# Kernel optimization log

Hardware: AMD Instinct MI355X
Metric: run time of the kernel (lower is better)

Reference implementation:

```python
import jax, jax.numpy as jnp
import numpy as np

DX = 1000.0
DY = 1000.0
EPS = 1e-8


def _weno5(qm2, qm1, q0, qp1, qp2):
    """Classic WENO5 left-biased reconstruction at the face i+1/2."""
    # candidate stencil reconstructions
    f1 = (1.0 / 3.0) * qm2 - (7.0 / 6.0) * qm1 + (11.0 / 6.0) * q0
    f2 = -(1.0 / 6.0) * qm1 + (5.0 / 6.0) * q0 + (1.0 / 3.0) * qp1
    f3 = (1.0 / 3.0) * q0 + (5.0 / 6.0) * qp1 - (1.0 / 6.0) * qp2
    # smoothness indicators
    k1, k2 = 13.0 / 12.0, 0.25
    b1 = k1 * (qm2 - 2.0 * qm1 + q0) ** 2 + k2 * (qm2 - 4.0 * qm1 + 3.0 * q0) ** 2
    b2 = k1 * (qm1 - 2.0 * q0 + qp1) ** 2 + k2 * (qm1 - qp1) ** 2
    b3 = k1 * (q0 - 2.0 * qp1 + qp2) ** 2 + k2 * (3.0 * q0 - 4.0 * qp1 + qp2) ** 2
    # nonlinear weights (ideal weights 1/10, 6/10, 3/10)
    w1 = 0.1 / (b1 + EPS) ** 2
    w2 = 0.6 / (b2 + EPS) ** 2
    w3 = 0.3 / (b3 + EPS) ** 2
    return (w1 * f1 + w2 * f2 + w3 * f3) / (w1 + w2 + w3)


def _flux_along(q, vel, axis):
    """Upwind WENO5 flux vel * q_face at faces i+1/2, one face per cell.

    fe[..., i] = flux at face between cells i and i+1 along `axis`.
    Boundary stencils use edge-replicated ghost cells.
    """
    n = q.shape[axis]
    pad = [(0, 0), (0, 0)]
    pad[axis] = (2, 3)  # left recon needs i-2..i+2, right recon needs i-1..i+3
    qp = jnp.pad(q, pad, mode='edge')

    def s(k):  # q at cell i+k, shape == q.shape
        return jax.lax.slice_in_dim(qp, 2 + k, 2 + k + n, axis=axis)

    q_left = _weno5(s(-2), s(-1), s(0), s(1), s(2))   # upwind for vel >= 0
    q_right = _weno5(s(3), s(2), s(1), s(0), s(-1))   # upwind for vel <  0 (mirrored)
    return vel * jnp.where(vel >= 0.0, q_left, q_right)


def setup_inputs() -> dict:
    key = jax.random.key(0)
    k1, k2, k3 = jax.random.split(key, 3)
    Ny, Nx = 2048, 4096
    h = jax.random.normal(k1, (Ny, Nx), dtype=jnp.float32)
    u = jax.random.normal(k2, (Ny, Nx), dtype=jnp.float32)
    v = jax.random.normal(k3, (Ny, Nx), dtype=jnp.float32)
    return {"h": h, "u": u, "v": v}


def reference(h, u, v):
    # WENO5 upwind fluxes at east (U-point) and north (V-point) faces
    fe = _flux_along(h, u, axis=1)
    fn = _flux_along(h, v, axis=0)
    # tendency -div(h u_vec) on the ghost=2 interior, zero on the ghost ring
    div = (fe[2:-2, 2:-2] - fe[2:-2, 1:-3]) / DX + (fn[2:-2, 2:-2] - fn[1:-3, 2:-2]) / DY
    out = jnp.zeros_like(h).at[2:-2, 2:-2].set(-div)
    return out
```

## Files before the change

kernel.cpp:

```cpp
#include <hip/hip_runtime.h>

#define NX 4096
#define NY 2048
#define EPS 1e-8f
#define ROWS 8
#define CPW 63
#define INV_D 0.001f

typedef float f32x2 __attribute__((ext_vector_type(2)));

__device__ __forceinline__ int clampi(int i, int lo, int hi) {
    return i < lo ? lo : (i > hi ? hi : i);
}

__device__ __forceinline__ float weno5_s(float qm2, float qm1, float q0,
                                         float qp1, float qp2) {
    float f1 = fmaf(1.0f/3.0f, qm2, fmaf(-7.0f/6.0f, qm1, (11.0f/6.0f)*q0));
    float f2 = fmaf(-1.0f/6.0f, qm1, fmaf(5.0f/6.0f, q0, (1.0f/3.0f)*qp1));
    float f3 = fmaf(1.0f/3.0f, q0, fmaf(5.0f/6.0f, qp1, (-1.0f/6.0f)*qp2));
    const float k1 = 13.0f/12.0f, k2 = 0.25f;
    float d1 = qm2 - 2.0f*qm1 + q0,  e1 = qm2 - 4.0f*qm1 + 3.0f*q0;
    float d2 = qm1 - 2.0f*q0 + qp1,  e2 = qm1 - qp1;
    float d3 = q0 - 2.0f*qp1 + qp2,  e3 = 3.0f*q0 - 4.0f*qp1 + qp2;
    float b1 = fmaf(k1, d1*d1, k2*(e1*e1));
    float b2 = fmaf(k1, d2*d2, k2*(e2*e2));
    float b3 = fmaf(k1, d3*d3, k2*(e3*e3));
    float t1 = b1 + EPS, t2 = b2 + EPS, t3 = b3 + EPS;
    float p23 = t2*t3, p13 = t1*t3, p12 = t1*t2;
    float w1 = 0.1f*(p23*p23), w2 = 0.6f*(p13*p13), w3 = 0.3f*(p12*p12);
    float num = fmaf(w1, f1, fmaf(w2, f2, w3*f3));
    return num * __builtin_amdgcn_rcpf((w1 + w2) + w3);
}

__device__ __forceinline__ f32x2 weno5_pk(f32x2 qm2, f32x2 qm1, f32x2 q0,
                                          f32x2 qp1, f32x2 qp2) {
    f32x2 f1 = (1.0f/3.0f)*qm2 - (7.0f/6.0f)*qm1 + (11.0f/6.0f)*q0;
    f32x2 f2 = (-1.0f/6.0f)*qm1 + (5.0f/6.0f)*q0 + (1.0f/3.0f)*qp1;
    f32x2 f3 = (1.0f/3.0f)*q0 + (5.0f/6.0f)*qp1 - (1.0f/6.0f)*qp2;
    f32x2 d1 = qm2 - 2.0f*qm1 + q0;
    f32x2 e1 = qm2 - 4.0f*qm1 + 3.0f*q0;
    f32x2 d2 = qm1 - 2.0f*q0 + qp1;
    f32x2 e2 = qm1 - qp1;
    f32x2 d3 = q0 - 2.0f*qp1 + qp2;
    f32x2 e3 = 3.0f*q0 - 4.0f*qp1 + qp2;
    const float k1 = 13.0f/12.0f, k2 = 0.25f;
    f32x2 b1 = k1*(d1*d1) + k2*(e1*e1);
    f32x2 b2 = k1*(d2*d2) + k2*(e2*e2);
    f32x2 b3 = k1*(d3*d3) + k2*(e3*e3);
    f32x2 t1 = b1 + EPS, t2 = b2 + EPS, t3 = b3 + EPS;
    f32x2 p23 = t2*t3, p13 = t1*t3, p12 = t1*t2;
    f32x2 w1 = 0.1f*(p23*p23);
    f32x2 w2 = 0.6f*(p13*p13);
    f32x2 w3 = 0.3f*(p12*p12);
    f32x2 num = w1*f1 + w2*f2 + w3*f3;
    f32x2 den = (w1 + w2) + w3;
    f32x2 rc;
    rc.x = __builtin_amdgcn_rcpf(den.x);
    rc.y = __builtin_amdgcn_rcpf(den.y);
    return num * rc;
}

template <bool EDGE>
__device__ __forceinline__ void run_strip(const float* __restrict__ h,
                                          const float* __restrict__ u,
                                          const float* __restrict__ v,
                                          float* __restrict__ out,
                                          int x0, int y0w, int lane) {
    const int xf = x0 - 1 + lane;
    const int xo = x0 + lane;
    const int xc = EDGE ? (xo < NX ? xo : NX - 1) : xo;
    const int xq = EDGE ? clampi(xf, 0, NX - 1) : xf;

    int xs[6];
    if (EDGE) {
#pragma unroll
        for (int k = 0; k < 6; ++k) xs[k] = clampi(xf - 2 + k, 0, NX - 1);
    }

    float col[ROWS + 6];
#pragma unroll
    for (int k = 0; k < ROWS + 6; ++k) {
        int yy = EDGE ? clampi(y0w - 3 + k, 0, NY - 1) : (y0w - 3 + k);
        col[k] = h[(size_t)yy * NX + xc];
    }
    float uu[ROWS];
#pragma unroll
    for (int r = 0; r < ROWS; ++r)
        uu[r] = u[(size_t)(y0w + r) * NX + xq];
    float vv[ROWS + 1];
#pragma unroll
    for (int j = 0; j <= ROWS; ++j) {
        int fy = EDGE ? clampi(y0w - 1 + j, 0, NY - 1) : (y0w - 1 + j);
        vv[j] = v[(size_t)fy * NX + xc];
    }
    float st[ROWS][6];
#pragma unroll
    for (int r = 0; r < ROWS; ++r) {
        const float* hr = h + (size_t)(y0w + r) * NX;
        if (EDGE) {
#pragma unroll
            for (int k = 0; k < 6; ++k) st[r][k] = hr[xs[k]];
        } else {
#pragma unroll
            for (int k = 0; k < 6; ++k) st[r][k] = hr[xf - 2 + k];
        }
    }

    float fn_prev;
    {
        float vl = vv[0];
        bool vp = (vl >= 0.0f);
        fn_prev = vl * weno5_s(vp ? col[0] : col[5], vp ? col[1] : col[4],
                               vp ? col[2] : col[3], vp ? col[3] : col[2],
                               vp ? col[4] : col[1]);
    }

#pragma unroll
    for (int r = 0; r < ROWS; ++r) {
        const int y = y0w + r;
        float uval = uu[r];
        float vval = vv[r + 1];
        bool up = (uval >= 0.0f);
        bool vp = (vval >= 0.0f);
        f32x2 a = { up ? st[r][0] : st[r][5], vp ? col[r+1] : col[r+6] };
        f32x2 b = { up ? st[r][1] : st[r][4], vp ? col[r+2] : col[r+5] };
        f32x2 c = { up ? st[r][2] : st[r][3], vp ? col[r+3] : col[r+4] };
        f32x2 d = { up ? st[r][3] : st[r][2], vp ? col[r+4] : col[r+3] };
        f32x2 e = { up ? st[r][4] : st[r][1], vp ? col[r+5] : col[r+2] };
        f32x2 q = weno5_pk(a, b, c, d, e);
        float fe = uval * q.x;
        float fn_cur = vval * q.y;
        float fe_r = __shfl_down(fe, 1);
        float val = ((fe - fe_r) + (fn_prev - fn_cur)) * INV_D;

        if (EDGE) {
            if (xo < 2 || xo >= NX - 2 || y < 2 || y >= NY - 2) val = 0.0f;
            if (lane < CPW && xo < NX)
                __builtin_nontemporal_store(val, out + (size_t)y * NX + xo);
        } else {
            if (lane < CPW)
                __builtin_nontemporal_store(val, out + (size_t)y * NX + xo);
        }
        fn_prev = fn_cur;
    }
}

__global__ __launch_bounds__(256) void adv_kernel(const float* __restrict__ h,
                                                  const float* __restrict__ u,
                                                  const float* __restrict__ v,
                                                  float* __restrict__ out) {
    const int lane = threadIdx.x & 63;
    const int wid  = threadIdx.x >> 6;
    const int x0 = blockIdx.x * CPW;
    const int y0w = (blockIdx.y * 4 + wid) * ROWS;

    const bool edge = (blockIdx.x == 0) || (blockIdx.x >= 64) ||
                      (blockIdx.y == 0) || (blockIdx.y == gridDim.y - 1);
    if (edge)
        run_strip<true>(h, u, v, out, x0, y0w, lane);
    else
        run_strip<false>(h, u, v, out, x0, y0w, lane);
}

extern "C" void kernel_launch(void* const* d_in, const int* in_sizes, int n_in,
                              void* d_out, int out_size, void* d_ws, size_t ws_size,
                              hipStream_t stream) {
    const float* h = (const float*)d_in[0];
    const float* u = (const float*)d_in[1];
    const float* v = (const float*)d_in[2];
    float* out = (float*)d_out;

    dim3 block(256, 1, 1);
    dim3 grid((NX + CPW - 1) / CPW, NY / (4 * ROWS), 1);
    adv_kernel<<<grid, block, 0, stream>>>(h, u, v, out);
}
```

Before: 38.88 us.

## Pair WENO evaluations by direction and software-pipeline row stencil loads

Replaces the old pairing, where each packed WENO call combined one x-face and one y-face, with same-direction pairs: all y-face fluxes are computed up front in packed pairs, and x-face fluxes are computed two rows at a time. Row stencil and u loads are double-buffered so the loads for the next row pair are issued while the current pair is being computed, instead of all loads landing before any compute. The aim is to hide memory latency and to cut the select logic needed per packed call. In exchange, register pressure may rise because all y fluxes are held in registers, and instruction scheduling changes.

```diff
diff --git a/kernel.cpp b/kernel.cpp
--- a/kernel.cpp
+++ b/kernel.cpp
@@ -77,71 +77,108 @@
         for (int k = 0; k < 6; ++k) xs[k] = clampi(xf - 2 + k, 0, NX - 1);
     }
 
-    float col[ROWS + 6];
+    float w[ROWS + 6];
 #pragma unroll
     for (int k = 0; k < ROWS + 6; ++k) {
         int yy = EDGE ? clampi(y0w - 3 + k, 0, NY - 1) : (y0w - 3 + k);
-        col[k] = h[(size_t)yy * NX + xc];
-    }
-    float uu[ROWS];
-#pragma unroll
-    for (int r = 0; r < ROWS; ++r)
-        uu[r] = u[(size_t)(y0w + r) * NX + xq];
+        w[k] = h[(size_t)yy * NX + xc];
+    }
     float vv[ROWS + 1];
 #pragma unroll
     for (int j = 0; j <= ROWS; ++j) {
         int fy = EDGE ? clampi(y0w - 1 + j, 0, NY - 1) : (y0w - 1 + j);
         vv[j] = v[(size_t)fy * NX + xc];
     }
-    float st[ROWS][6];
-#pragma unroll
-    for (int r = 0; r < ROWS; ++r) {
-        const float* hr = h + (size_t)(y0w + r) * NX;
+
+    float st[4][2][6];
+    float uu[4][2];
+
+#pragma unroll
+    for (int i = 0; i < 2; ++i) {
+        const float* hr = h + (size_t)(y0w + i) * NX;
         if (EDGE) {
 #pragma unroll
-            for (int k = 0; k < 6; ++k) st[r][k] = hr[xs[k]];
+            for (int k = 0; k < 6; ++k) st[0][i][k] = hr[xs[k]];
         } else {
 #pragma unroll
-            for (int k = 0; k < 6; ++k) st[r][k] = hr[xf - 2 + k];
+            for (int k = 0; k < 6; ++k) st[0][i][k] = hr[xf - 2 + k];
         }
-    }
-
-    float fn_prev;
+        uu[0][i] = u[(size_t)(y0w + i) * NX + xq];
+    }
+
+    float fn[ROWS + 1];
+#pragma unroll
+    for (int j = 0; j < ROWS; j += 2) {
+        float v0 = vv[j], v1 = vv[j + 1];
+        bool p0 = (v0 >= 0.0f), p1 = (v1 >= 0.0f);
+        f32x2 a = { p0 ? w[j]   : w[j+5], p1 ? w[j+1] : w[j+6] };
+        f32x2 b = { p0 ? w[j+1] : w[j+4], p1 ? w[j+2] : w[j+5] };
+        f32x2 c = { p0 ? w[j+2] : w[j+3], p1 ? w[j+3] : w[j+4] };
+        f32x2 d = { p0 ? w[j+3] : w[j+2], p1 ? w[j+4] : w[j+3] };
+        f32x2 e = { p0 ? w[j+4] : w[j+1], p1 ? w[j+5] : w[j+2] };
+        f32x2 q = weno5_pk(a, b, c, d, e);
+        fn[j] = v0 * q.x;
+        fn[j + 1] = v1 * q.y;
+    }
     {
-        float vl = vv[0];
+        float vl = vv[ROWS];
         bool vp = (vl >= 0.0f);
-        fn_prev = vl * weno5_s(vp ? col[0] : col[5], vp ? col[1] : col[4],
-                               vp ? col[2] : col[3], vp ? col[3] : col[2],
-                               vp ? col[4] : col[1]);
-    }
-
-#pragma unroll
-    for (int r = 0; r < ROWS; ++r) {
-        const int y = y0w + r;
-        float uval = uu[r];
-        float vval = vv[r + 1];
-        bool up = (uval >= 0.0f);
-        bool vp = (vval >= 0.0f);
-        f32x2 a = { up ? st[r][0] : st[r][5], vp ? col[r+1] : col[r+6] };
-        f32x2 b = { up ? st[r][1] : st[r][4], vp ? col[r+2] : col[r+5] };
-        f32x2 c = { up ? st[r][2] : st[r][3], vp ? col[r+3] : col[r+4] };
-        f32x2 d = { up ? st[r][3] : st[r][2], vp ? col[r+4] : col[r+3] };
-        f32x2 e = { up ? st[r][4] : st[r][1], vp ? col[r+5] : col[r+2] };
+        fn[ROWS] = vl * weno5_s(vp ? w[ROWS]   : w[ROWS+5],
+                                vp ? w[ROWS+1] : w[ROWS+4],
+                                vp ? w[ROWS+2] : w[ROWS+3],
+                                vp ? w[ROWS+3] : w[ROWS+2],
+                                vp ? w[ROWS+4] : w[ROWS+1]);
+    }
+
+#pragma unroll
+    for (int p = 0; p < 4; ++p) {
+        if (p < 3) {
+#pragma unroll
+            for (int i = 0; i < 2; ++i) {
+                int y = y0w + 2 * (p + 1) + i;
+                const float* hr = h + (size_t)y * NX;
+                if (EDGE) {
+#pragma unroll
+                    for (int k = 0; k < 6; ++k) st[p+1][i][k] = hr[xs[k]];
+                } else {
+#pragma unroll
+                    for (int k = 0; k < 6; ++k) st[p+1][i][k] = hr[xf - 2 + k];
+                }
+                uu[p+1][i] = u[(size_t)y * NX + xq];
+            }
+        }
+
+        float u0 = uu[p][0], u1 = uu[p][1];
+        bool q0p = (u0 >= 0.0f), q1p = (u1 >= 0.0f);
+        f32x2 a = { q0p ? st[p][0][0] : st[p][0][5], q1p ? st[p][1][0] : st[p][1][5] };
+        f32x2 b = { q0p ? st[p][0][1] : st[p][0][4], q1p ? st[p][1][1] : st[p][1][4] };
+        f32x2 c = { q0p ? st[p][0][2] : st[p][0][3], q1p ? st[p][1][2] : st[p][1][3] };
+        f32x2 d = { q0p ? st[p][0][3] : st[p][0][2], q1p ? st[p][1][3] : st[p][1][2] };
+        f32x2 e = { q0p ? st[p][0][4] : st[p][0][1], q1p ? st[p][1][4] : st[p][1][1] };
         f32x2 q = weno5_pk(a, b, c, d, e);
-        float fe = uval * q.x;
-        float fn_cur = vval * q.y;
-        float fe_r = __shfl_down(fe, 1);
-        float val = ((fe - fe_r) + (fn_prev - fn_cur)) * INV_D;
-
+        float fe0 = u0 * q.x;
+        float fe1 = u1 * q.y;
+        float fe0r = __shfl_down(fe0, 1);
+        float fe1r = __shfl_down(fe1, 1);
+
+        int r0 = 2 * p;
+        float val0 = ((fe0 - fe0r) + (fn[r0]     - fn[r0 + 1])) * INV_D;
+        float val1 = ((fe1 - fe1r) + (fn[r0 + 1] - fn[r0 + 2])) * INV_D;
+
+        int y0r = y0w + r0;
         if (EDGE) {
-            if (xo < 2 || xo >= NX - 2 || y < 2 || y >= NY - 2) val = 0.0f;
-            if (lane < CPW && xo < NX)
-                __builtin_nontemporal_store(val, out + (size_t)y * NX + xo);
+            if (xo < 2 || xo >= NX - 2 || y0r < 2 || y0r >= NY - 2) val0 = 0.0f;
+            if (xo < 2 || xo >= NX - 2 || y0r + 1 < 2 || y0r + 1 >= NY - 2) val1 = 0.0f;
+            if (lane < CPW && xo < NX) {
+                __builtin_nontemporal_store(val0, out + (size_t)y0r * NX + xo);
+                __builtin_nontemporal_store(val1, out + (size_t)(y0r + 1) * NX + xo);
+            }
         } else {
-            if (lane < CPW)
-                __builtin_nontemporal_store(val, out + (size_t)y * NX + xo);
+            if (lane < CPW) {
+                __builtin_nontemporal_store(val0, out + (size_t)y0r * NX + xo);
+                __builtin_nontemporal_store(val1, out + (size_t)(y0r + 1) * NX + xo);
+            }
         }
-        fn_prev = fn_cur;
     }
 }
 
```

After: 39.24 us. No clear change (+0.9%).

## Load interior h row once per lane and build x-stencil with cross-lane shuffles

Applied to the files above, without the earlier changes.

The interior path now loads a single h value per lane per row (offset by three columns) and builds the six-point x-stencil and the center column from wavefront shuffles, replacing six separate global loads per row. To keep enough halo lanes for the shifted window, columns per wave drop from 63 to 56, and the edge predicate is updated to match. This cuts load instructions and cache traffic in exchange for more shuffle (ds_bpermute) work and a larger grid with more redundant halo lanes.

```diff
diff --git a/kernel.cpp b/kernel.cpp
--- a/kernel.cpp
+++ b/kernel.cpp
@@ -4,7 +4,7 @@
 #define NY 2048
 #define EPS 1e-8f
 #define ROWS 8
-#define CPW 63
+#define CPW 56
 #define INV_D 0.001f
 
 typedef float f32x2 __attribute__((ext_vector_type(2)));
@@ -60,50 +60,114 @@
     return num * rc;
 }
 
-template <bool EDGE>
-__device__ __forceinline__ void run_strip(const float* __restrict__ h,
-                                          const float* __restrict__ u,
-                                          const float* __restrict__ v,
-                                          float* __restrict__ out,
-                                          int x0, int y0w, int lane) {
+__device__ __forceinline__ void run_int(const float* __restrict__ h,
+                                        const float* __restrict__ u,
+                                        const float* __restrict__ v,
+                                        float* __restrict__ out,
+                                        int x0, int y0w, int lane) {
+    const int xh = x0 - 3 + lane;
+    const int xq = x0 - 1 + lane;
+    const int xc = x0 + lane;
+
+    float hv[ROWS];
+#pragma unroll
+    for (int r = 0; r < ROWS; ++r)
+        hv[r] = h[(size_t)(y0w + r) * NX + xh];
+    float col[ROWS + 6];
+#pragma unroll
+    for (int k = 0; k < 3; ++k) {
+        col[k] = h[(size_t)(y0w - 3 + k) * NX + xc];
+        col[ROWS + 3 + k] = h[(size_t)(y0w + ROWS + k) * NX + xc];
+    }
+    float uu[ROWS];
+#pragma unroll
+    for (int r = 0; r < ROWS; ++r)
+        uu[r] = u[(size_t)(y0w + r) * NX + xq];
+    float vv[ROWS + 1];
+#pragma unroll
+    for (int j = 0; j <= ROWS; ++j)
+        vv[j] = v[(size_t)(y0w - 1 + j) * NX + xc];
+
+#pragma unroll
+    for (int r = 0; r < ROWS; ++r)
+        col[3 + r] = __shfl(hv[r], lane + 3);
+
+    float fn_prev;
+    {
+        float vl = vv[0];
+        bool vp = (vl >= 0.0f);
+        fn_prev = vl * weno5_s(vp ? col[0] : col[5], vp ? col[1] : col[4],
+                               vp ? col[2] : col[3], vp ? col[3] : col[2],
+                               vp ? col[4] : col[1]);
+    }
+
+#pragma unroll
+    for (int r = 0; r < ROWS; ++r) {
+        const int y = y0w + r;
+        float s0 = hv[r];
+        float s1 = __shfl(hv[r], lane + 1);
+        float s2 = __shfl(hv[r], lane + 2);
+        float s3 = col[r + 3];
+        float s4 = __shfl(hv[r], lane + 4);
+        float s5 = __shfl(hv[r], lane + 5);
+
+        float uval = uu[r];
+        float vval = vv[r + 1];
+        bool up = (uval >= 0.0f);
+        bool vp = (vval >= 0.0f);
+        f32x2 a = { up ? s0 : s5, vp ? col[r+1] : col[r+6] };
+        f32x2 b = { up ? s1 : s4, vp ? col[r+2] : col[r+5] };
+        f32x2 c = { up ? s2 : s3, vp ? col[r+3] : col[r+4] };
+        f32x2 d = { up ? s3 : s2, vp ? col[r+4] : col[r+3] };
+        f32x2 e = { up ? s4 : s1, vp ? col[r+5] : col[r+2] };
+        f32x2 q = weno5_pk(a, b, c, d, e);
+        float fe = uval * q.x;
+        float fn_cur = vval * q.y;
+        float fe_r = __shfl_down(fe, 1);
+        float val = ((fe - fe_r) + (fn_prev - fn_cur)) * INV_D;
+
+        if (lane < CPW)
+            __builtin_nontemporal_store(val, out + (size_t)y * NX + xc);
+        fn_prev = fn_cur;
+    }
+}
+
+__device__ __forceinline__ void run_edge(const float* __restrict__ h,
+                                         const float* __restrict__ u,
+                                         const float* __restrict__ v,
+                                         float* __restrict__ out,
+                                         int x0, int y0w, int lane) {
     const int xf = x0 - 1 + lane;
     const int xo = x0 + lane;
-    const int xc = EDGE ? (xo < NX ? xo : NX - 1) : xo;
-    const int xq = EDGE ? clampi(xf, 0, NX - 1) : xf;
+    const int xc = xo < NX ? xo : NX - 1;
+    const int xq = clampi(xf, 0, NX - 1);
 
     int xs[6];
-    if (EDGE) {
-#pragma unroll
-        for (int k = 0; k < 6; ++k) xs[k] = clampi(xf - 2 + k, 0, NX - 1);
-    }
+#pragma unroll
+    for (int k = 0; k < 6; ++k) xs[k] = clampi(xf - 2 + k, 0, NX - 1);
 
     float col[ROWS + 6];
 #pragma unroll
     for (int k = 0; k < ROWS + 6; ++k) {
-        int yy = EDGE ? clampi(y0w - 3 + k, 0, NY - 1) : (y0w - 3 + k);
+        int yy = clampi(y0w - 3 + k, 0, NY - 1);
         col[k] = h[(size_t)yy * NX + xc];
     }
+    float vv[ROWS + 1];
+#pragma unroll
+    for (int j = 0; j <= ROWS; ++j) {
+        int fy = clampi(y0w - 1 + j, 0, NY - 1);
+        vv[j] = v[(size_t)fy * NX + xc];
+    }
     float uu[ROWS];
 #pragma unroll
     for (int r = 0; r < ROWS; ++r)
         uu[r] = u[(size_t)(y0w + r) * NX + xq];
-    float vv[ROWS + 1];
-#pragma unroll
-    for (int j = 0; j <= ROWS; ++j) {
-        int fy = EDGE ? clampi(y0w - 1 + j, 0, NY - 1) : (y0w - 1 + j);
-        vv[j] = v[(size_t)fy * NX + xc];
-    }
     float st[ROWS][6];
 #pragma unroll
     for (int r = 0; r < ROWS; ++r) {
         const float* hr = h + (size_t)(y0w + r) * NX;
-        if (EDGE) {
-#pragma unroll
-            for (int k = 0; k < 6; ++k) st[r][k] = hr[xs[k]];
-        } else {
-#pragma unroll
-            for (int k = 0; k < 6; ++k) st[r][k] = hr[xf - 2 + k];
-        }
+#pragma unroll
+        for (int k = 0; k < 6; ++k) st[r][k] = hr[xs[k]];
     }
 
     float fn_prev;
@@ -131,16 +195,11 @@
         float fe = uval * q.x;
         float fn_cur = vval * q.y;
         float fe_r = __shfl_down(fe, 1);
-        float val = ((fe - fe_r) + (fn_prev - fn_cur)) * INV_D;
-
-        if (EDGE) {
-            if (xo < 2 || xo >= NX - 2 || y < 2 || y >= NY - 2) val = 0.0f;
-            if (lane < CPW && xo < NX)
-                __builtin_nontemporal_store(val, out + (size_t)y * NX + xo);
-        } else {
-            if (lane < CPW)
-                __builtin_nontemporal_store(val, out + (size_t)y * NX + xo);
-        }
+        float val = 0.0f;
+        if (xo >= 2 && xo < NX - 2 && y >= 2 && y < NY - 2)
+            val = ((fe - fe_r) + (fn_prev - fn_cur)) * INV_D;
+        if (lane < CPW && xo < NX)
+            __builtin_nontemporal_store(val, out + (size_t)y * NX + xo);
         fn_prev = fn_cur;
     }
 }
@@ -154,12 +213,12 @@
     const int x0 = blockIdx.x * CPW;
     const int y0w = (blockIdx.y * 4 + wid) * ROWS;
 
-    const bool edge = (blockIdx.x == 0) || (blockIdx.x >= 64) ||
+    const bool edge = (blockIdx.x == 0) || (blockIdx.x >= (NX / CPW)) ||
                       (blockIdx.y == 0) || (blockIdx.y == gridDim.y - 1);
     if (edge)
-        run_strip<true>(h, u, v, out, x0, y0w, lane);
+        run_edge(h, u, v, out, x0, y0w, lane);
     else
-        run_strip<false>(h, u, v, out, x0, y0w, lane);
+        run_int(h, u, v, out, x0, y0w, lane);
 }
 
 extern "C" void kernel_launch(void* const* d_in, const int* in_sizes, int n_in,
```

Result: slower. 40.58 us (+4.4%).
